# Optimization experiments

Hardware: AMD Instinct MI355X
Metric: run time of the kernel (lower is better)

## Reference

```python
import jax, jax.numpy as jnp
import numpy as np

N_NODES = 100000
N_EDGES = 1600000
D_IN = 128
D_HID = 256
D_OUT = 128


def setup_inputs() -> dict:
    key = jax.random.key(0)
    ks = jax.random.split(key, 8)
    x = jax.random.normal(ks[0], (N_NODES, D_IN), dtype=jnp.float32)
    edge_vals = jax.random.uniform(ks[1], (N_EDGES,), dtype=jnp.float32)
    # MLP params, scaled for numerical stability (fan-in style)
    W1 = jax.random.normal(ks[2], (D_IN, D_HID), dtype=jnp.float32) / np.sqrt(D_IN)
    b1 = jnp.zeros((D_HID,), dtype=jnp.float32)
    W2 = jax.random.normal(ks[3], (D_HID, D_OUT), dtype=jnp.float32) / np.sqrt(D_HID)
    b2 = jnp.zeros((D_OUT,), dtype=jnp.float32)
    eps = jnp.zeros((1,), dtype=jnp.float32)
    edge_src = jax.random.randint(ks[4], (N_EDGES,), 0, N_NODES, dtype=jnp.int32)
    edge_dst = jax.random.randint(ks[5], (N_EDGES,), 0, N_NODES, dtype=jnp.int32)
    return {
        "x": x, "edge_vals": edge_vals,
        "W1": W1, "b1": b1, "W2": W2, "b2": b2,
        "eps": eps, "edge_src": edge_src, "edge_dst": edge_dst,
    }


def reference(x, edge_vals, W1, b1, W2, b2, eps, edge_src, edge_dst):
    # Sparse SpMM: AX = A @ x with A in COO (dst <- val * x[src]).
    # dropout_rate=0 -> identity; single support matrix.
    gathered = edge_vals[:, None] * x[edge_src]            # [E, D_in]
    AX = jax.ops.segment_sum(gathered, edge_dst, num_segments=x.shape[0])  # [N, D_in]
    # GIN self-loop combine
    h = AX + (1.0 + eps) * x                                # [N, D_in]
    # MLP_for_GIN (2 layers): Linear -> ReLU -> Linear
    h = jax.nn.relu(h @ W1 + b1)                            # [N, D_hid]
    out = h @ W2 + b2                                       # [N, D_out]
    # act_func=None -> no final activation
    return out
```

## Files before the change

### kernel.cpp

```cpp
#include <hip/hip_runtime.h>
#include <hip/hip_bf16.h>

typedef __attribute__((ext_vector_type(8))) __bf16 bf16x8;
typedef __attribute__((ext_vector_type(4))) float f32x4;

#define NN 100000
#define NE 1600000
#define NBK 6250
#define ECHUNK 200000
#define CELL 96
#define MAXE 1024
#define GB 2048

__device__ __forceinline__ float bflo(unsigned w) { return __uint_as_float(w << 16); }
__device__ __forceinline__ float bfhi(unsigned w) { return __uint_as_float(w & 0xffff0000u); }

__global__ __launch_bounds__(256) void front_kernel(const float* __restrict__ W1,
                                                    const float* __restrict__ W2,
                                                    __bf16* __restrict__ W1T,
                                                    __bf16* __restrict__ W2T,
                                                    const float4* __restrict__ x4,
                                                    uint2* __restrict__ xb,
                                                    const int* __restrict__ esrc,
                                                    const int* __restrict__ edst,
                                                    const float* __restrict__ ev,
                                                    int* __restrict__ cnt8,
                                                    int2* __restrict__ pairs) {
    const int b = blockIdx.x, t = threadIdx.x;
    if (b < 128) {
        int tid = b * 256 + t;
        int k1 = tid >> 8, n1 = tid & 255;
        W1T[n1 * 128 + k1] = (__bf16)W1[tid];
        int k2 = tid >> 7, n2 = tid & 127;
        W2T[n2 * 256 + k2] = (__bf16)W2[tid];
    }
    for (int i = b * 256 + t; i < NN * 32; i += GB * 256) {
        float4 v = x4[i];
        __bf16 b0 = (__bf16)v.x, b1 = (__bf16)v.y, b2 = (__bf16)v.z, b3 = (__bf16)v.w;
        uint2 o;
        o.x = (unsigned)*(unsigned short*)&b0 | ((unsigned)*(unsigned short*)&b1 << 16);
        o.y = (unsigned)*(unsigned short*)&b2 | ((unsigned)*(unsigned short*)&b3 << 16);
        xb[i] = o;
    }
    {
        int grp = b & 7, blk = b >> 3, nblk = GB >> 3;
        int* cnt = cnt8 + grp * NBK;
        int lo = grp * ECHUNK, hi = lo + ECHUNK;
        if (hi > NE) hi = NE;
        for (int e = lo + blk * 256 + t; e < hi; e += nblk * 256) {
            int d = edst[e];
            int s = esrc[e];
            float v = ev[e];
            int bk = d >> 4;
            int c = atomicAdd(&cnt[bk], 1);
            if (c < CELL) {
                int2 p; p.x = (s << 8) | (d & 15); p.y = __float_as_int(v);
                pairs[(size_t)(bk * 8 + grp) * CELL + c] = p;
            }
        }
    }
}

__global__ __launch_bounds__(1024) void sort_gather_kernel(const unsigned* __restrict__ xb,
                                                           const int* __restrict__ cnt8,
                                                           const int2* __restrict__ pairs,
                                                           const float* __restrict__ eps,
                                                           uint2* __restrict__ AXb) {
    __shared__ int2 raw[MAXE];
    __shared__ int2 srt[MAXE];
    __shared__ int rcnt[16], rofs[16], rcur[16];

    const int t = threadIdx.x;
    const int b = blockIdx.x;
    const int wave = t >> 6, lane = t & 63;
    const unsigned hw = lane >> 5, l32 = lane & 31u;
    const char* xbase = (const char*)xb + l32 * 8;

    int m = 0, mypref = 0, mylen = 0;
#pragma unroll
    for (int g = 0; g < 8; ++g) {
        int len = cnt8[g * NBK + b];
        len = (len < 0) ? 0 : ((len > CELL) ? CELL : len);
        if (g == wave) { mypref = m; mylen = len; }
        m += len;
    }
    if (t < 16) rcnt[t] = 0;
    __syncthreads();
    if (wave < 8) {
        const size_t segbase = (size_t)(b * 8 + wave) * CELL;
        for (int i = lane; i < mylen; i += 64)
            raw[mypref + i] = pairs[segbase + i];
    }
    __syncthreads();
    for (int i = t; i < m; i += 1024)
        atomicAdd(&rcnt[raw[i].x & 15], 1);
    __syncthreads();
    if (t == 0) {
        int run = 0;
#pragma unroll
        for (int r = 0; r < 16; ++r) { rofs[r] = run; rcur[r] = run; run += rcnt[r]; }
    }
    __syncthreads();
    for (int i = t; i < m; i += 1024) {
        int2 p = raw[i];
        int pos = atomicAdd(&rcur[p.x & 15], 1);
        int2 q; q.x = p.x & 0xffffff00; q.y = p.y;
        srt[pos] = q;
    }
    __syncthreads();

    float a0 = 0.f, a1 = 0.f, a2 = 0.f, a3 = 0.f;
    {
        const int je = rofs[wave] + rcnt[wave];
        int j = rofs[wave] + (int)hw;
        for (; j + 6 < je; j += 8) {
            int2 e0 = srt[j], e1 = srt[j + 2], e2 = srt[j + 4], e3 = srt[j + 6];
            uint2 w0 = *(const uint2*)(xbase + e0.x);
            uint2 w1 = *(const uint2*)(xbase + e1.x);
            uint2 w2 = *(const uint2*)(xbase + e2.x);
            uint2 w3 = *(const uint2*)(xbase + e3.x);
            float v0 = __int_as_float(e0.y), v1 = __int_as_float(e1.y);
            float v2 = __int_as_float(e2.y), v3 = __int_as_float(e3.y);
            a0 = fmaf(v0, bflo(w0.x), a0); a1 = fmaf(v0, bfhi(w0.x), a1);
            a2 = fmaf(v0, bflo(w0.y), a2); a3 = fmaf(v0, bfhi(w0.y), a3);
            a0 = fmaf(v1, bflo(w1.x), a0); a1 = fmaf(v1, bfhi(w1.x), a1);
            a2 = fmaf(v1, bflo(w1.y), a2); a3 = fmaf(v1, bfhi(w1.y), a3);
            a0 = fmaf(v2, bflo(w2.x), a0); a1 = fmaf(v2, bfhi(w2.x), a1);
            a2 = fmaf(v2, bflo(w2.y), a2); a3 = fmaf(v2, bfhi(w2.y), a3);
            a0 = fmaf(v3, bflo(w3.x), a0); a1 = fmaf(v3, bfhi(w3.x), a1);
            a2 = fmaf(v3, bflo(w3.y), a2); a3 = fmaf(v3, bfhi(w3.y), a3);
        }
        for (; j < je; j += 2) {
            int2 e0 = srt[j];
            uint2 w0 = *(const uint2*)(xbase + e0.x);
            float v0 = __int_as_float(e0.y);
            a0 = fmaf(v0, bflo(w0.x), a0); a1 = fmaf(v0, bfhi(w0.x), a1);
            a2 = fmaf(v0, bflo(w0.y), a2); a3 = fmaf(v0, bfhi(w0.y), a3);
        }
    }

    a0 += __shfl_xor(a0, 32); a1 += __shfl_xor(a1, 32);
    a2 += __shfl_xor(a2, 32); a3 += __shfl_xor(a3, 32);
    if (hw == 0) {
        const int n = b * 16 + wave;
        uint2 ws = *(const uint2*)(xbase + (size_t)n * 256);
        float sc = 1.0f + eps[0];
        a0 = fmaf(sc, bflo(ws.x), a0); a1 = fmaf(sc, bfhi(ws.x), a1);
        a2 = fmaf(sc, bflo(ws.y), a2); a3 = fmaf(sc, bfhi(ws.y), a3);
        __bf16 b0 = (__bf16)a0, b1 = (__bf16)a1, b2 = (__bf16)a2, b3 = (__bf16)a3;
        uint2 o;
        o.x = (unsigned)*(unsigned short*)&b0 | ((unsigned)*(unsigned short*)&b1 << 16);
        o.y = (unsigned)*(unsigned short*)&b2 | ((unsigned)*(unsigned short*)&b3 << 16);
        AXb[(size_t)n * 32 + l32] = o;
    }
}

__global__ void convert_w_kernel(const float* __restrict__ W1, const float* __restrict__ W2,
                                 __bf16* __restrict__ W1T, __bf16* __restrict__ W2T) {
    int tid = blockIdx.x * 256 + threadIdx.x;
    if (tid < 128 * 256) {
        int k1 = tid >> 8, n1 = tid & 255;
        W1T[n1 * 128 + k1] = (__bf16)W1[tid];
        int k2 = tid >> 7, n2 = tid & 127;
        W2T[n2 * 256 + k2] = (__bf16)W2[tid];
    }
}

__global__ void init_ax_kernel(const float4* __restrict__ x, float4* __restrict__ AX,
                               const float* __restrict__ eps, int n4) {
    int i = blockIdx.x * blockDim.x + threadIdx.x;
    if (i >= n4) return;
    float s = 1.0f + eps[0];
    float4 v = x[i];
    v.x *= s; v.y *= s; v.z *= s; v.w *= s;
    AX[i] = v;
}

__global__ void scatter_kernel(const float2* __restrict__ x2, const float* __restrict__ ev,
                               const int* __restrict__ esrc, const int* __restrict__ edst,
                               float* AX) {
    unsigned gid = blockIdx.x * 256u + threadIdx.x;
    unsigned e = gid >> 6;
    unsigned lane = gid & 63u;
    if (e >= NE) return;
    float v = ev[e];
    int s = esrc[e], d = edst[e];
    float2 xv = x2[(size_t)s * 64 + lane];
    float* dstp = AX + (size_t)d * 128 + lane * 2;
    atomicAdd(dstp,     v * xv.x);
    atomicAdd(dstp + 1, v * xv.y);
}

template <typename AT>
__global__ __launch_bounds__(256) void mlp_kernel(const AT* A,
                                                  const __bf16* __restrict__ W1T,
                                                  const __bf16* __restrict__ W2T,
                                                  const float* __restrict__ b1,
                                                  const float* __restrict__ b2,
                                                  float* out) {
    __shared__ __bf16 Hl[64][264];

    const int wave = threadIdx.x >> 6;
    const int lane = threadIdx.x & 63;
    const int l15  = lane & 15;
    const int lhi  = lane >> 4;
    const int rowbase = blockIdx.x * 64;

    f32x4 acc1[4][4] = {};
#pragma unroll
    for (int ks = 0; ks < 4; ++ks) {
        const int k0 = ks * 32 + lhi * 8;
        bf16x8 am[4], bn[4];
#pragma unroll
        for (int mt = 0; mt < 4; ++mt) {
            int row = rowbase + mt * 16 + l15;
            if (row >= NN) row = NN - 1;
            if constexpr (__is_same(AT, __bf16)) {
                am[mt] = *(const bf16x8*)(A + (size_t)row * 128 + k0);
            } else {
                const float4* ap = (const float4*)(A + (size_t)row * 128 + k0);
                float4 f0 = ap[0], f1 = ap[1];
                bf16x8 a;
                a[0]=(__bf16)f0.x; a[1]=(__bf16)f0.y; a[2]=(__bf16)f0.z; a[3]=(__bf16)f0.w;
                a[4]=(__bf16)f1.x; a[5]=(__bf16)f1.y; a[6]=(__bf16)f1.z; a[7]=(__bf16)f1.w;
                am[mt] = a;
            }
        }
#pragma unroll
        for (int nt = 0; nt < 4; ++nt) {
            int n = wave * 64 + nt * 16 + l15;
            bn[nt] = *(const bf16x8*)(W1T + (size_t)n * 128 + k0);
        }
#pragma unroll
        for (int mt = 0; mt < 4; ++mt)
#pragma unroll
            for (int nt = 0; nt < 4; ++nt)
                acc1[mt][nt] = __builtin_amdgcn_mfma_f32_16x16x32_bf16(am[mt], bn[nt], acc1[mt][nt], 0, 0, 0);
    }

#pragma unroll
    for (int nt = 0; nt < 4; ++nt) {
        int n = wave * 64 + nt * 16 + l15;
        float bias = b1[n];
#pragma unroll
        for (int mt = 0; mt < 4; ++mt)
#pragma unroll
            for (int r = 0; r < 4; ++r) {
                float h = acc1[mt][nt][r] + bias;
                Hl[mt * 16 + lhi * 4 + r][n] = (__bf16)fmaxf(h, 0.0f);
            }
    }
    __syncthreads();

    f32x4 acc2[4][2] = {};
#pragma unroll
    for (int ks = 0; ks < 8; ++ks) {
        const int k0 = ks * 32 + lhi * 8;
        bf16x8 ha[4], wb[2];
#pragma unroll
        for (int mt = 0; mt < 4; ++mt)
            ha[mt] = *(const bf16x8*)(&Hl[mt * 16 + l15][k0]);
#pragma unroll
        for (int nt = 0; nt < 2; ++nt) {
            int n = wave * 32 + nt * 16 + l15;
            wb[nt] = *(const bf16x8*)(W2T + (size_t)n * 256 + k0);
        }
#pragma unroll
        for (int mt = 0; mt < 4; ++mt)
#pragma unroll
            for (int nt = 0; nt < 2; ++nt)
                acc2[mt][nt] = __builtin_amdgcn_mfma_f32_16x16x32_bf16(ha[mt], wb[nt], acc2[mt][nt], 0, 0, 0);
    }

#pragma unroll
    for (int nt = 0; nt < 2; ++nt) {
        int n = wave * 32 + nt * 16 + l15;
        float bias = b2[n];
#pragma unroll
        for (int mt = 0; mt < 4; ++mt)
#pragma unroll
            for (int r = 0; r < 4; ++r) {
                int row = rowbase + mt * 16 + lhi * 4 + r;
                if (row < NN) out[(size_t)row * 128 + n] = acc2[mt][nt][r] + bias;
            }
    }
}

extern "C" void kernel_launch(void* const* d_in, const int* in_sizes, int n_in,
                              void* d_out, int out_size, void* d_ws, size_t ws_size,
                              hipStream_t stream) {
    const float* x    = (const float*)d_in[0];
    const float* ev   = (const float*)d_in[1];
    const float* W1   = (const float*)d_in[2];
    const float* b1   = (const float*)d_in[3];
    const float* W2   = (const float*)d_in[4];
    const float* b2   = (const float*)d_in[5];
    const float* eps  = (const float*)d_in[6];
    const int*   esrc = (const int*)d_in[7];
    const int*   edst = (const int*)d_in[8];
    float* out = (float*)d_out;

    char* ws = (char*)d_ws;
    size_t off = 0;
    auto alloc = [&](size_t bytes) { void* p = ws + off; off += (bytes + 511) & ~size_t(511); return p; };

    __bf16* W1T   = (__bf16*)alloc(128 * 256 * sizeof(__bf16));
    __bf16* W2T   = (__bf16*)alloc(128 * 256 * sizeof(__bf16));
    int* cnt8     = (int*)  alloc((size_t)8 * NBK * sizeof(int));
    int2* pairs   = (int2*) alloc((size_t)NBK * 8 * CELL * sizeof(int2));
    unsigned* xb  = (unsigned*)alloc((size_t)NN * 64 * sizeof(unsigned));
    unsigned* AXb = (unsigned*)alloc((size_t)NN * 64 * sizeof(unsigned));
    bool csr_ok = (off <= ws_size);

    if (csr_ok) {
        hipMemsetAsync(cnt8, 0, (size_t)8 * NBK * sizeof(int), stream);
        front_kernel<<<GB, 256, 0, stream>>>(W1, W2, W1T, W2T, (const float4*)x,
                                             (uint2*)xb, esrc, edst, ev, cnt8, pairs);
        sort_gather_kernel<<<NBK, 1024, 0, stream>>>(xb, cnt8, pairs, eps, (uint2*)AXb);
        int nblk = (NN + 63) / 64;
        mlp_kernel<__bf16><<<nblk, 256, 0, stream>>>((const __bf16*)AXb, W1T, W2T, b1, b2, out);
    } else {
        __bf16* W1Tf = (__bf16*)ws;
        __bf16* W2Tf = W1Tf + 128 * 256;
        convert_w_kernel<<<128, 256, 0, stream>>>(W1, W2, W1Tf, W2Tf);
        int n4 = NN * 128 / 4;
        init_ax_kernel<<<(n4 + 255) / 256, 256, 0, stream>>>((const float4*)x, (float4*)out, eps, n4);
        scatter_kernel<<<(NE * 64u) / 256u, 256, 0, stream>>>((const float2*)x, ev, esrc, edst, out);
        int nblk = (NN + 63) / 64;
        mlp_kernel<float><<<nblk, 256, 0, stream>>>(out, W1Tf, W2Tf, b1, b2, out);
    }
}
```

Before: 211.4 us.

## Replace global-atomic edge bucketing with two-pass LDS-aggregated radix partition

Edge binning into 16-node buckets used one global atomic per edge across 8 groups. It now runs in two passes. First, each block bins its chunk of edges into 49 super-buckets, using LDS counters and one global atomic per super-bucket per block. A new refine kernel then splits each super-bucket into 128 sub-buckets the same way. This sharply cuts global atomic contention but adds an extra kernel launch and an extra read and write of all edge pairs. Fixed capacities (CAPA, CAPB) silently drop edges if a bucket overflows, and the src index shift leaves fewer bits for node ids.

```diff
diff --git a/kernel.cpp b/kernel.cpp
--- a/kernel.cpp
+++ b/kernel.cpp
@@ -7,15 +7,17 @@
 #define NN 100000
 #define NE 1600000
 #define NBK 6250
-#define ECHUNK 200000
-#define CELL 96
-#define MAXE 1024
-#define GB 2048
+#define SUP 49
+#define CAPA 36864
+#define EPB 2048
+#define NBA 782
+#define NSLC 16
+#define CAPB 384
 
 __device__ __forceinline__ float bflo(unsigned w) { return __uint_as_float(w << 16); }
 __device__ __forceinline__ float bfhi(unsigned w) { return __uint_as_float(w & 0xffff0000u); }
 
-__global__ __launch_bounds__(256) void front_kernel(const float* __restrict__ W1,
+__global__ __launch_bounds__(512) void front_kernel(const float* __restrict__ W1,
                                                     const float* __restrict__ W2,
                                                     __bf16* __restrict__ W1T,
                                                     __bf16* __restrict__ W2T,
@@ -24,17 +26,19 @@
                                                     const int* __restrict__ esrc,
                                                     const int* __restrict__ edst,
                                                     const float* __restrict__ ev,
-                                                    int* __restrict__ cnt8,
-                                                    int2* __restrict__ pairs) {
+                                                    int* __restrict__ supercnt,
+                                                    int2* __restrict__ psup) {
+    __shared__ int scnt[SUP], sbase[SUP], scur[SUP];
     const int b = blockIdx.x, t = threadIdx.x;
-    if (b < 128) {
-        int tid = b * 256 + t;
+
+    if (b < 64) {
+        int tid = b * 512 + t;
         int k1 = tid >> 8, n1 = tid & 255;
         W1T[n1 * 128 + k1] = (__bf16)W1[tid];
         int k2 = tid >> 7, n2 = tid & 127;
         W2T[n2 * 256 + k2] = (__bf16)W2[tid];
     }
-    for (int i = b * 256 + t; i < NN * 32; i += GB * 256) {
+    for (int i = b * 512 + t; i < NN * 32; i += NBA * 512) {
         float4 v = x4[i];
         __bf16 b0 = (__bf16)v.x, b1 = (__bf16)v.y, b2 = (__bf16)v.z, b3 = (__bf16)v.w;
         uint2 o;
@@ -42,32 +46,71 @@
         o.y = (unsigned)*(unsigned short*)&b2 | ((unsigned)*(unsigned short*)&b3 << 16);
         xb[i] = o;
     }
-    {
-        int grp = b & 7, blk = b >> 3, nblk = GB >> 3;
-        int* cnt = cnt8 + grp * NBK;
-        int lo = grp * ECHUNK, hi = lo + ECHUNK;
-        if (hi > NE) hi = NE;
-        for (int e = lo + blk * 256 + t; e < hi; e += nblk * 256) {
-            int d = edst[e];
-            int s = esrc[e];
-            float v = ev[e];
-            int bk = d >> 4;
-            int c = atomicAdd(&cnt[bk], 1);
-            if (c < CELL) {
-                int2 p; p.x = (s << 8) | (d & 15); p.y = __float_as_int(v);
-                pairs[(size_t)(bk * 8 + grp) * CELL + c] = p;
-            }
-        }
+    const int lo = b * EPB;
+    const int hi = (lo + EPB < NE) ? lo + EPB : NE;
+    if (t < SUP) scnt[t] = 0;
+    __syncthreads();
+    for (int e = lo + t; e < hi; e += 512)
+        atomicAdd(&scnt[edst[e] >> 11], 1);
+    __syncthreads();
+    if (t < SUP) {
+        int c = scnt[t];
+        sbase[t] = c ? atomicAdd(&supercnt[t], c) : 0;
+        scur[t] = 0;
+    }
+    __syncthreads();
+    for (int e = lo + t; e < hi; e += 512) {
+        int d = edst[e];
+        int s = esrc[e];
+        float v = ev[e];
+        int sp = d >> 11;
+        int off = sbase[sp] + atomicAdd(&scur[sp], 1);
+        if (off < CAPA) {
+            int2 p; p.x = (s << 11) | (d & 0x7FF); p.y = __float_as_int(v);
+            psup[(size_t)sp * CAPA + off] = p;
+        }
+    }
+}
+
+__global__ __launch_bounds__(512) void refine_kernel(const int2* __restrict__ psup,
+                                                     const int* __restrict__ supercnt,
+                                                     int* __restrict__ bktcnt,
+                                                     int2* __restrict__ pairs2) {
+    __shared__ int lcnt[128], lbase[128], lcur[128];
+    const int s = blockIdx.x / NSLC, sl = blockIdx.x % NSLC, t = threadIdx.x;
+    int cnt = supercnt[s]; if (cnt > CAPA) cnt = CAPA;
+    const int per = (cnt + NSLC - 1) / NSLC;
+    const int beg = sl * per;
+    const int end = (beg + per < cnt) ? beg + per : cnt;
+    const int2* seg = psup + (size_t)s * CAPA;
+
+    if (t < 128) lcnt[t] = 0;
+    __syncthreads();
+    for (int i = beg + t; i < end; i += 512)
+        atomicAdd(&lcnt[(seg[i].x >> 4) & 127], 1);
+    __syncthreads();
+    if (t < 128) {
+        int c = lcnt[t];
+        lbase[t] = c ? atomicAdd(&bktcnt[(s << 7) + t], c) : 0;
+        lcur[t] = 0;
+    }
+    __syncthreads();
+    for (int i = beg + t; i < end; i += 512) {
+        int2 p = seg[i];
+        int sub = (p.x >> 4) & 127;
+        int off = lbase[sub] + atomicAdd(&lcur[sub], 1);
+        if (off < CAPB)
+            pairs2[(size_t)((s << 7) + sub) * CAPB + off] = p;
     }
 }
 
 __global__ __launch_bounds__(1024) void sort_gather_kernel(const unsigned* __restrict__ xb,
-                                                           const int* __restrict__ cnt8,
-                                                           const int2* __restrict__ pairs,
+                                                           const int* __restrict__ bktcnt,
+                                                           const int2* __restrict__ pairs2,
                                                            const float* __restrict__ eps,
                                                            uint2* __restrict__ AXb) {
-    __shared__ int2 raw[MAXE];
-    __shared__ int2 srt[MAXE];
+    __shared__ int2 raw[CAPB];
+    __shared__ int2 srt[CAPB];
     __shared__ int rcnt[16], rofs[16], rcur[16];
 
     const int t = threadIdx.x;
@@ -76,24 +119,16 @@
     const unsigned hw = lane >> 5, l32 = lane & 31u;
     const char* xbase = (const char*)xb + l32 * 8;
 
-    int m = 0, mypref = 0, mylen = 0;
-#pragma unroll
-    for (int g = 0; g < 8; ++g) {
-        int len = cnt8[g * NBK + b];
-        len = (len < 0) ? 0 : ((len > CELL) ? CELL : len);
-        if (g == wave) { mypref = m; mylen = len; }
-        m += len;
-    }
+    int m = bktcnt[b]; if (m > CAPB) m = CAPB;
+    const int2* seg = pairs2 + (size_t)b * CAPB;
+
     if (t < 16) rcnt[t] = 0;
     __syncthreads();
-    if (wave < 8) {
-        const size_t segbase = (size_t)(b * 8 + wave) * CELL;
-        for (int i = lane; i < mylen; i += 64)
-            raw[mypref + i] = pairs[segbase + i];
-    }
-    __syncthreads();
-    for (int i = t; i < m; i += 1024)
-        atomicAdd(&rcnt[raw[i].x & 15], 1);
+    for (int i = t; i < m; i += 1024) {
+        int2 p = seg[i];
+        raw[i] = p;
+        atomicAdd(&rcnt[p.x & 15], 1);
+    }
     __syncthreads();
     if (t == 0) {
         int run = 0;
@@ -104,7 +139,8 @@
     for (int i = t; i < m; i += 1024) {
         int2 p = raw[i];
         int pos = atomicAdd(&rcur[p.x & 15], 1);
-        int2 q; q.x = p.x & 0xffffff00; q.y = p.y;
+        int2 q; q.x = (p.x >> 3) & 0xFFFFFF00;
+        q.y = p.y;
         srt[pos] = q;
     }
     __syncthreads();
@@ -306,17 +342,21 @@
 
     __bf16* W1T   = (__bf16*)alloc(128 * 256 * sizeof(__bf16));
     __bf16* W2T   = (__bf16*)alloc(128 * 256 * sizeof(__bf16));
-    int* cnt8     = (int*)  alloc((size_t)8 * NBK * sizeof(int));
-    int2* pairs   = (int2*) alloc((size_t)NBK * 8 * CELL * sizeof(int2));
+    int* cnts     = (int*)  alloc((size_t)(SUP + NBK) * sizeof(int));
+    int2* psup    = (int2*) alloc((size_t)SUP * CAPA * sizeof(int2));
+    int2* pairs2  = (int2*) alloc((size_t)NBK * CAPB * sizeof(int2));
     unsigned* xb  = (unsigned*)alloc((size_t)NN * 64 * sizeof(unsigned));
     unsigned* AXb = (unsigned*)alloc((size_t)NN * 64 * sizeof(unsigned));
     bool csr_ok = (off <= ws_size);
 
     if (csr_ok) {
-        hipMemsetAsync(cnt8, 0, (size_t)8 * NBK * sizeof(int), stream);
-        front_kernel<<<GB, 256, 0, stream>>>(W1, W2, W1T, W2T, (const float4*)x,
-                                             (uint2*)xb, esrc, edst, ev, cnt8, pairs);
-        sort_gather_kernel<<<NBK, 1024, 0, stream>>>(xb, cnt8, pairs, eps, (uint2*)AXb);
+        int* supercnt = cnts;
+        int* bktcnt   = cnts + SUP;
+        hipMemsetAsync(cnts, 0, (size_t)(SUP + NBK) * sizeof(int), stream);
+        front_kernel<<<NBA, 512, 0, stream>>>(W1, W2, W1T, W2T, (const float4*)x,
+                                              (uint2*)xb, esrc, edst, ev, supercnt, psup);
+        refine_kernel<<<SUP * NSLC, 512, 0, stream>>>(psup, supercnt, bktcnt, pairs2);
+        sort_gather_kernel<<<NBK, 1024, 0, stream>>>(xb, bktcnt, pairs2, eps, (uint2*)AXb);
         int nblk = (NN + 63) / 64;
         mlp_kernel<__bf16><<<nblk, 256, 0, stream>>>((const __bf16*)AXb, W1T, W2T, b1, b2, out);
     } else {
```

After: 178.0 us. 1.19x faster.
